# Optimization experiments

Hardware: AMD Instinct MI355X
Metric: run time of the kernel (lower is better)

The kernel has to match this reference:

```python
import jax, jax.numpy as jnp
import numpy as np

B, T, I, H, O = 256, 512, 128, 256, 1


def setup_inputs() -> dict:
    key = jax.random.key(0)
    ks = jax.random.split(key, 7)
    s_ih = 1.0 / np.sqrt(H)
    return {
        "x": jax.random.normal(ks[0], (B, T, I), dtype=jnp.float32),
        "W_ih": jax.random.uniform(ks[1], (H, I), jnp.float32, -s_ih, s_ih),
        "W_hh": jax.random.uniform(ks[2], (H, H), jnp.float32, -s_ih, s_ih),
        "b_ih": jax.random.uniform(ks[3], (H,), jnp.float32, -s_ih, s_ih),
        "b_hh": jax.random.uniform(ks[4], (H,), jnp.float32, -s_ih, s_ih),
        "fc_w": jax.random.uniform(ks[5], (O, H), jnp.float32, -s_ih, s_ih),
        "fc_b": jax.random.uniform(ks[6], (O,), jnp.float32, -s_ih, s_ih),
    }


def reference(x, W_ih, W_hh, b_ih, b_hh, fc_w, fc_b):
    # Elman RNN (tanh), batch_first, single layer, h0 = zeros.
    # Only the last hidden state feeds the fc head, so scan carries h only.
    b = b_ih + b_hh
    xW = jnp.einsum('bti,hi->tbh', x, W_ih) + b  # precompute input projection [T,B,H]

    def step(h, xw_t):
        h = jnp.tanh(xw_t + h @ W_hh.T)
        return h, None

    h0 = jnp.zeros((x.shape[0], W_hh.shape[0]), dtype=x.dtype)
    h_last, _ = jax.lax.scan(step, h0, xW)
    return h_last @ fc_w.T + fc_b  # [B, O]
```

## Files before the change

### kernel.cpp

```cpp
#include <hip/hip_runtime.h>
#include <hip/hip_bf16.h>

#define B_ 256
#define T_ 512
#define I_ 128
#define H_ 256

#define SC 2.885390081777927f

typedef __bf16 bf16x8 __attribute__((ext_vector_type(8)));
typedef float  f32x4  __attribute__((ext_vector_type(4)));
typedef unsigned short u16;
typedef unsigned int   u32;

union U16x8Cast { uint4 v; bf16x8 b; };

__device__ inline u16 f2b(float f) {
    union { __bf16 h; u16 u; } c; c.h = (__bf16)f; return c.u;
}
__device__ inline bf16x8 pack8(float4 lo, float4 hi) {
    bf16x8 f;
    f[0]=(__bf16)lo.x; f[1]=(__bf16)lo.y; f[2]=(__bf16)lo.z; f[3]=(__bf16)lo.w;
    f[4]=(__bf16)hi.x; f[5]=(__bf16)hi.y; f[6]=(__bf16)hi.z; f[7]=(__bf16)hi.w;
    return f;
}
__device__ inline bf16x8 pack8s(float4 lo, float4 hi, float s) {
    bf16x8 f;
    f[0]=(__bf16)(lo.x*s); f[1]=(__bf16)(lo.y*s); f[2]=(__bf16)(lo.z*s); f[3]=(__bf16)(lo.w*s);
    f[4]=(__bf16)(hi.x*s); f[5]=(__bf16)(hi.y*s); f[6]=(__bf16)(hi.z*s); f[7]=(__bf16)(hi.w*s);
    return f;
}
__device__ inline uint2 pack4(float a, float b, float c, float d) {
    uint2 p;
    p.x = (u32)f2b(a) | ((u32)f2b(b) << 16);
    p.y = (u32)f2b(c) | ((u32)f2b(d) << 16);
    return p;
}
__device__ inline f32x4 b4_to_f32x4(uint2 u) {
    f32x4 r;
    r[0] = __uint_as_float(u.x << 16);
    r[1] = __uint_as_float(u.x & 0xFFFF0000u);
    r[2] = __uint_as_float(u.y << 16);
    r[3] = __uint_as_float(u.y & 0xFFFF0000u);
    return r;
}
__device__ inline float tanh_pre(float s) {
    float e = __builtin_amdgcn_exp2f(s);
    float r = __builtin_amdgcn_rcpf(1.f + e);
    return fmaf(-2.f, r, 1.f);
}

#define WG_BARRIER() asm volatile("s_waitcnt lgkmcnt(0)\n\ts_barrier" ::: "memory")

#define LDST 264
__global__ __launch_bounds__(256, 2) void xw_gemm_mfma(const float* __restrict__ x,
                                                       const float* __restrict__ W_ih,
                                                       const float* __restrict__ b_ih,
                                                       const float* __restrict__ b_hh,
                                                       u16* __restrict__ xw) {
    __shared__ u16 tile[64 * LDST];

    const int tid  = (int)threadIdx.x;
    const int wave = tid >> 6;
    const int lane = tid & 63;
    const int q    = lane >> 4;
    const int ml   = lane & 15;
    const int m0   = (int)blockIdx.x * 128;
    const int b    = m0 >> 9;
    const int t0   = m0 & 511;
    const int n0   = wave * 64;

    bf16x8 wA[4][4];
#pragma unroll
    for (int tau = 0; tau < 4; ++tau) {
        const float* wr = W_ih + (size_t)(n0 + tau * 16 + ml) * I_;
#pragma unroll
        for (int kap = 0; kap < 4; ++kap) {
            const int k0 = kap * 32 + q * 8;
            wA[tau][kap] = pack8s(*(const float4*)(wr + k0), *(const float4*)(wr + k0 + 4), SC);
        }
    }

    f32x4 acc[8][4];
#pragma unroll
    for (int mt = 0; mt < 8; ++mt)
#pragma unroll
        for (int tau = 0; tau < 4; ++tau) acc[mt][tau] = (f32x4)0.f;

#pragma unroll
    for (int kap = 0; kap < 4; ++kap) {
        bf16x8 xB[8];
#pragma unroll
        for (int mt = 0; mt < 8; ++mt) {
            const float* xr = x + (size_t)(m0 + mt * 16 + ml) * I_ + kap * 32 + q * 8;
            xB[mt] = pack8(*(const float4*)xr, *(const float4*)(xr + 4));
        }
#pragma unroll
        for (int mt = 0; mt < 8; ++mt)
#pragma unroll
            for (int tau = 0; tau < 4; ++tau)
                acc[mt][tau] = __builtin_amdgcn_mfma_f32_16x16x32_bf16(
                    wA[tau][kap], xB[mt], acc[mt][tau], 0, 0, 0);
    }

    float4 bias4[4];
#pragma unroll
    for (int tau = 0; tau < 4; ++tau) {
        const int n = n0 + tau * 16 + q * 4;
        float4 bi = *(const float4*)(b_ih + n);
        float4 bh = *(const float4*)(b_hh + n);
        bias4[tau] = make_float4((bi.x + bh.x) * SC, (bi.y + bh.y) * SC,
                                 (bi.z + bh.z) * SC, (bi.w + bh.w) * SC);
    }

#pragma unroll
    for (int p = 0; p < 2; ++p) {
        if (p) __syncthreads();
#pragma unroll
        for (int mt = 0; mt < 4; ++mt) {
            const int row = mt * 16 + ml;
            const int mg  = p * 4 + mt;
#pragma unroll
            for (int tau = 0; tau < 4; ++tau) {
                uint2 pk = pack4(acc[mg][tau][0] + bias4[tau].x,
                                 acc[mg][tau][1] + bias4[tau].y,
                                 acc[mg][tau][2] + bias4[tau].z,
                                 acc[mg][tau][3] + bias4[tau].w);
                *(uint2*)(tile + row * LDST + n0 + tau * 16 + q * 4) = pk;
            }
        }
        __syncthreads();
#pragma unroll
        for (int s = 0; s < 4; ++s) {
            const int rr = s * 16 + (tid >> 4);
            const int c  = tid & 15;
            const uint4* srcp = (const uint4*)(tile + rr * LDST);
            uint4* dstp = (uint4*)(xw + ((size_t)(t0 + p * 64 + rr) * B_ + b) * H_);
            uint4 v0 = srcp[c];
            uint4 v1 = srcp[c + 16];
            dstp[c] = v0;
            dstp[c + 16] = v1;
        }
    }
}

__global__ __launch_bounds__(512, 2) void rnn_scan_mfma(const u16* __restrict__ xw,
                                                        const float* __restrict__ W_hh,
                                                        const float* __restrict__ fc_w,
                                                        const float* __restrict__ fc_b,
                                                        float* __restrict__ out) {
    __shared__ __attribute__((aligned(16))) u16 hbuf[2][4096];
    __shared__ float red[8][16];

    const int tid  = (int)threadIdx.x;
    const int wave = tid >> 6;
    const int lane = tid & 63;
    const int q    = lane >> 4;
    const int m    = lane & 15;
    const int b0   = (int)blockIdx.x * 16;

    bf16x8 wf[2][8];
#pragma unroll
    for (int tau2 = 0; tau2 < 2; ++tau2) {
        const float* wr = W_hh + (size_t)(wave * 32 + tau2 * 16 + m) * H_;
#pragma unroll
        for (int kap = 0; kap < 8; ++kap) {
            const int k0 = kap * 32 + q * 8;
            wf[tau2][kap] = pack8s(*(const float4*)(wr + k0), *(const float4*)(wr + k0 + 4), SC);
        }
    }

    int widx[2];
#pragma unroll
    for (int tau2 = 0; tau2 < 2; ++tau2) {
        const int nbw = wave * 32 + tau2 * 16 + q * 4;
        widx[tau2] = (nbw >> 5) * 512 + (((nbw >> 3) & 3) * 16 + m) * 8 + (nbw & 7);
    }

    {
        uint4* p = (uint4*)&hbuf[0][0];
        const uint4 z = {0u, 0u, 0u, 0u};
        p[tid] = z;
    }
    WG_BARRIER();

    const u16* xwp = xw + (size_t)(b0 + m) * H_ + (wave * 32 + q * 4);
    const size_t tstride = (size_t)B_ * H_;

    uint2 pfA[2], pfB[2];
    pfA[0] = *(const uint2*)(xwp);
    pfA[1] = *(const uint2*)(xwp + 16);
    pfB[0] = *(const uint2*)(xwp + tstride);
    pfB[1] = *(const uint2*)(xwp + tstride + 16);

    int cur = 0;
    f32x4 acc[2];
    for (int tt = 0; tt < T_ / 2; ++tt) {
        {
            const int t = 2 * tt;
            acc[0] = b4_to_f32x4(pfA[0]);
            acc[1] = b4_to_f32x4(pfA[1]);
            if (t + 2 < T_) {
                const u16* pt = xwp + (size_t)(t + 2) * tstride;
                pfA[0] = *(const uint2*)(pt);
                pfA[1] = *(const uint2*)(pt + 16);
            }
            const uint4* hb = (const uint4*)&hbuf[cur][0];
#pragma unroll
            for (int kap = 0; kap < 8; ++kap) {
                U16x8Cast c; c.v = hb[kap * 64 + lane];
                acc[0] = __builtin_amdgcn_mfma_f32_16x16x32_bf16(wf[0][kap], c.b, acc[0], 0, 0, 0);
                acc[1] = __builtin_amdgcn_mfma_f32_16x16x32_bf16(wf[1][kap], c.b, acc[1], 0, 0, 0);
            }
            u16* wb = &hbuf[cur ^ 1][0];
#pragma unroll
            for (int tau2 = 0; tau2 < 2; ++tau2) {
                uint2 pk = pack4(tanh_pre(acc[tau2][0]), tanh_pre(acc[tau2][1]),
                                 tanh_pre(acc[tau2][2]), tanh_pre(acc[tau2][3]));
                *(uint2*)(wb + widx[tau2]) = pk;
            }
            WG_BARRIER();
            cur ^= 1;
        }
        {
            const int t = 2 * tt + 1;
            acc[0] = b4_to_f32x4(pfB[0]);
            acc[1] = b4_to_f32x4(pfB[1]);
            if (t + 2 < T_) {
                const u16* pt = xwp + (size_t)(t + 2) * tstride;
                pfB[0] = *(const uint2*)(pt);
                pfB[1] = *(const uint2*)(pt + 16);
            }
            const uint4* hb = (const uint4*)&hbuf[cur][0];
#pragma unroll
            for (int kap = 0; kap < 8; ++kap) {
                U16x8Cast c; c.v = hb[kap * 64 + lane];
                acc[0] = __builtin_amdgcn_mfma_f32_16x16x32_bf16(wf[0][kap], c.b, acc[0], 0, 0, 0);
                acc[1] = __builtin_amdgcn_mfma_f32_16x16x32_bf16(wf[1][kap], c.b, acc[1], 0, 0, 0);
            }
            if (t != T_ - 1) {
                u16* wb = &hbuf[cur ^ 1][0];
#pragma unroll
                for (int tau2 = 0; tau2 < 2; ++tau2) {
                    uint2 pk = pack4(tanh_pre(acc[tau2][0]), tanh_pre(acc[tau2][1]),
                                     tanh_pre(acc[tau2][2]), tanh_pre(acc[tau2][3]));
                    *(uint2*)(wb + widx[tau2]) = pk;
                }
                WG_BARRIER();
                cur ^= 1;
            }
        }
    }

    float4 fcw[2];
#pragma unroll
    for (int tau2 = 0; tau2 < 2; ++tau2)
        fcw[tau2] = *(const float4*)(fc_w + wave * 32 + tau2 * 16 + q * 4);

    float partial = 0.f;
#pragma unroll
    for (int tau2 = 0; tau2 < 2; ++tau2) {
        partial += tanh_pre(acc[tau2][0]) * fcw[tau2].x;
        partial += tanh_pre(acc[tau2][1]) * fcw[tau2].y;
        partial += tanh_pre(acc[tau2][2]) * fcw[tau2].z;
        partial += tanh_pre(acc[tau2][3]) * fcw[tau2].w;
    }
    partial += __shfl_xor(partial, 16);
    partial += __shfl_xor(partial, 32);
    __syncthreads();
    if (lane < 16) red[wave][m] = partial;
    __syncthreads();
    if (tid < 16) {
        float s = red[0][tid] + red[1][tid] + red[2][tid] + red[3][tid]
                + red[4][tid] + red[5][tid] + red[6][tid] + red[7][tid];
        out[b0 + tid] = s + fc_b[0];
    }
}

extern "C" void kernel_launch(void* const* d_in, const int* in_sizes, int n_in,
                              void* d_out, int out_size, void* d_ws, size_t ws_size,
                              hipStream_t stream) {
    const float* x    = (const float*)d_in[0];
    const float* W_ih = (const float*)d_in[1];
    const float* W_hh = (const float*)d_in[2];
    const float* b_ih = (const float*)d_in[3];
    const float* b_hh = (const float*)d_in[4];
    const float* fc_w = (const float*)d_in[5];
    const float* fc_b = (const float*)d_in[6];
    float* out = (float*)d_out;

    u16* xwbuf = (u16*)d_ws;
    xw_gemm_mfma<<<(B_ * T_) / 128, 256, 0, stream>>>(x, W_ih, b_ih, b_hh, xwbuf);
    rnn_scan_mfma<<<B_ / 16, 512, 0, stream>>>(xwbuf, W_hh, fc_w, fc_b, out);
}
```

Measured before the change: 370.0 us.

## Process two batch groups per block to interleave independent MFMA chains

Each scan block now handles 32 batch rows as two 16-row groups, with separate LDS hidden-state buffers and accumulators. Both groups share the register-resident W_hh fragments and one barrier per timestep. Their independent MFMA dependency chains can overlap to hide latency in the serial recurrence. In exchange each step does more work per wave, register pressure rises (launch bounds lowered to one block), and the grid halves.

```diff
diff --git a/kernel.cpp b/kernel.cpp
--- a/kernel.cpp
+++ b/kernel.cpp
@@ -144,20 +144,20 @@
     }
 }
 
-__global__ __launch_bounds__(512, 2) void rnn_scan_mfma(const u16* __restrict__ xw,
+__global__ __launch_bounds__(512, 1) void rnn_scan_mfma(const u16* __restrict__ xw,
                                                         const float* __restrict__ W_hh,
                                                         const float* __restrict__ fc_w,
                                                         const float* __restrict__ fc_b,
                                                         float* __restrict__ out) {
-    __shared__ __attribute__((aligned(16))) u16 hbuf[2][4096];
-    __shared__ float red[8][16];
+    __shared__ __attribute__((aligned(16))) u16 hbuf[2][2][4096];
+    __shared__ float red[2][8][16];
 
     const int tid  = (int)threadIdx.x;
     const int wave = tid >> 6;
     const int lane = tid & 63;
     const int q    = lane >> 4;
     const int m    = lane & 15;
-    const int b0   = (int)blockIdx.x * 16;
+    const int b0   = (int)blockIdx.x * 32;
 
     bf16x8 wf[2][8];
 #pragma unroll
@@ -178,102 +178,111 @@
     }
 
     {
-        uint4* p = (uint4*)&hbuf[0][0];
         const uint4 z = {0u, 0u, 0u, 0u};
-        p[tid] = z;
-    }
-    WG_BARRIER();
-
-    const u16* xwp = xw + (size_t)(b0 + m) * H_ + (wave * 32 + q * 4);
+        ((uint4*)&hbuf[0][0][0])[tid] = z;
+        ((uint4*)&hbuf[1][0][0])[tid] = z;
+    }
+    __syncthreads();
+
+    const u16* xwpA = xw + (size_t)(b0 + m) * H_ + (wave * 32 + q * 4);
+    const u16* xwpB = xwpA + (size_t)16 * H_;
     const size_t tstride = (size_t)B_ * H_;
 
-    uint2 pfA[2], pfB[2];
-    pfA[0] = *(const uint2*)(xwp);
-    pfA[1] = *(const uint2*)(xwp + 16);
-    pfB[0] = *(const uint2*)(xwp + tstride);
-    pfB[1] = *(const uint2*)(xwp + tstride + 16);
+    uint2 pfEA[2], pfOA[2], pfEB[2], pfOB[2];
+    pfEA[0] = *(const uint2*)(xwpA);             pfEA[1] = *(const uint2*)(xwpA + 16);
+    pfEB[0] = *(const uint2*)(xwpB);             pfEB[1] = *(const uint2*)(xwpB + 16);
+    pfOA[0] = *(const uint2*)(xwpA + tstride);   pfOA[1] = *(const uint2*)(xwpA + tstride + 16);
+    pfOB[0] = *(const uint2*)(xwpB + tstride);   pfOB[1] = *(const uint2*)(xwpB + tstride + 16);
 
     int cur = 0;
-    f32x4 acc[2];
+    f32x4 accA[2], accB[2];
+
+#define DUAL_STEP(T_CUR, PFA, PFB, WRITE_OUT)                                   \
+    {                                                                           \
+        const int t_ = (T_CUR);                                                 \
+            \
+        const uint4* hbA_ = (const uint4*)&hbuf[0][cur][0];                     \
+        const uint4* hbB_ = (const uint4*)&hbuf[1][cur][0];                     \
+        U16x8Cast cvA[8], cvB[8];                                               \
+        _Pragma("unroll")                                                       \
+        for (int k = 0; k < 8; ++k) cvA[k].v = hbA_[k * 64 + lane];             \
+        _Pragma("unroll")                                                       \
+        for (int k = 0; k < 8; ++k) cvB[k].v = hbB_[k * 64 + lane];             \
+                    \
+        accA[0] = b4_to_f32x4(PFA[0]);  accA[1] = b4_to_f32x4(PFA[1]);          \
+        accB[0] = b4_to_f32x4(PFB[0]);  accB[1] = b4_to_f32x4(PFB[1]);          \
+        if (t_ + 2 < T_) {                                                      \
+            const u16* ptA_ = xwpA + (size_t)(t_ + 2) * tstride;                \
+            const u16* ptB_ = xwpB + (size_t)(t_ + 2) * tstride;                \
+            PFA[0] = *(const uint2*)(ptA_);  PFA[1] = *(const uint2*)(ptA_ + 16); \
+            PFB[0] = *(const uint2*)(ptB_);  PFB[1] = *(const uint2*)(ptB_ + 16); \
+        }                                                                       \
+                      \
+        _Pragma("unroll")                                                       \
+        for (int k = 0; k < 8; ++k) {                                           \
+            accA[0] = __builtin_amdgcn_mfma_f32_16x16x32_bf16(wf[0][k], cvA[k].b, accA[0], 0, 0, 0); \
+            accA[1] = __builtin_amdgcn_mfma_f32_16x16x32_bf16(wf[1][k], cvA[k].b, accA[1], 0, 0, 0); \
+        }                                                                       \
+        _Pragma("unroll")                                                       \
+        for (int k = 0; k < 8; ++k) {                                           \
+            accB[0] = __builtin_amdgcn_mfma_f32_16x16x32_bf16(wf[0][k], cvB[k].b, accB[0], 0, 0, 0); \
+            accB[1] = __builtin_amdgcn_mfma_f32_16x16x32_bf16(wf[1][k], cvB[k].b, accB[1], 0, 0, 0); \
+        }                                                                       \
+           \
+        if (WRITE_OUT) {                                                        \
+            u16* wbA_ = &hbuf[0][cur ^ 1][0];                                   \
+            u16* wbB_ = &hbuf[1][cur ^ 1][0];                                   \
+            _Pragma("unroll")                                                   \
+            for (int tau2 = 0; tau2 < 2; ++tau2) {                              \
+                uint2 pk_ = pack4(tanh_pre(accA[tau2][0]), tanh_pre(accA[tau2][1]), \
+                                  tanh_pre(accA[tau2][2]), tanh_pre(accA[tau2][3])); \
+                *(uint2*)(wbA_ + widx[tau2]) = pk_;                             \
+            }                                                                   \
+            _Pragma("unroll")                                                   \
+            for (int tau2 = 0; tau2 < 2; ++tau2) {                              \
+                uint2 pk_ = pack4(tanh_pre(accB[tau2][0]), tanh_pre(accB[tau2][1]), \
+                                  tanh_pre(accB[tau2][2]), tanh_pre(accB[tau2][3])); \
+                *(uint2*)(wbB_ + widx[tau2]) = pk_;                             \
+            }                                                                   \
+            WG_BARRIER();                                                       \
+            cur ^= 1;                                                           \
+        }                                                                       \
+    }
+
     for (int tt = 0; tt < T_ / 2; ++tt) {
-        {
-            const int t = 2 * tt;
-            acc[0] = b4_to_f32x4(pfA[0]);
-            acc[1] = b4_to_f32x4(pfA[1]);
-            if (t + 2 < T_) {
-                const u16* pt = xwp + (size_t)(t + 2) * tstride;
-                pfA[0] = *(const uint2*)(pt);
-                pfA[1] = *(const uint2*)(pt + 16);
-            }
-            const uint4* hb = (const uint4*)&hbuf[cur][0];
-#pragma unroll
-            for (int kap = 0; kap < 8; ++kap) {
-                U16x8Cast c; c.v = hb[kap * 64 + lane];
-                acc[0] = __builtin_amdgcn_mfma_f32_16x16x32_bf16(wf[0][kap], c.b, acc[0], 0, 0, 0);
-                acc[1] = __builtin_amdgcn_mfma_f32_16x16x32_bf16(wf[1][kap], c.b, acc[1], 0, 0, 0);
-            }
-            u16* wb = &hbuf[cur ^ 1][0];
-#pragma unroll
-            for (int tau2 = 0; tau2 < 2; ++tau2) {
-                uint2 pk = pack4(tanh_pre(acc[tau2][0]), tanh_pre(acc[tau2][1]),
-                                 tanh_pre(acc[tau2][2]), tanh_pre(acc[tau2][3]));
-                *(uint2*)(wb + widx[tau2]) = pk;
-            }
-            WG_BARRIER();
-            cur ^= 1;
-        }
-        {
-            const int t = 2 * tt + 1;
-            acc[0] = b4_to_f32x4(pfB[0]);
-            acc[1] = b4_to_f32x4(pfB[1]);
-            if (t + 2 < T_) {
-                const u16* pt = xwp + (size_t)(t + 2) * tstride;
-                pfB[0] = *(const uint2*)(pt);
-                pfB[1] = *(const uint2*)(pt + 16);
-            }
-            const uint4* hb = (const uint4*)&hbuf[cur][0];
-#pragma unroll
-            for (int kap = 0; kap < 8; ++kap) {
-                U16x8Cast c; c.v = hb[kap * 64 + lane];
-                acc[0] = __builtin_amdgcn_mfma_f32_16x16x32_bf16(wf[0][kap], c.b, acc[0], 0, 0, 0);
-                acc[1] = __builtin_amdgcn_mfma_f32_16x16x32_bf16(wf[1][kap], c.b, acc[1], 0, 0, 0);
-            }
-            if (t != T_ - 1) {
-                u16* wb = &hbuf[cur ^ 1][0];
-#pragma unroll
-                for (int tau2 = 0; tau2 < 2; ++tau2) {
-                    uint2 pk = pack4(tanh_pre(acc[tau2][0]), tanh_pre(acc[tau2][1]),
-                                     tanh_pre(acc[tau2][2]), tanh_pre(acc[tau2][3]));
-                    *(uint2*)(wb + widx[tau2]) = pk;
-                }
-                WG_BARRIER();
-                cur ^= 1;
-            }
-        }
-    }
+        DUAL_STEP(2 * tt,     pfEA, pfEB, true);
+        DUAL_STEP(2 * tt + 1, pfOA, pfOB, (2 * tt + 1) != (T_ - 1));
+    }
+#undef DUAL_STEP
 
     float4 fcw[2];
 #pragma unroll
     for (int tau2 = 0; tau2 < 2; ++tau2)
         fcw[tau2] = *(const float4*)(fc_w + wave * 32 + tau2 * 16 + q * 4);
 
-    float partial = 0.f;
+    float pA = 0.f, pB = 0.f;
 #pragma unroll
     for (int tau2 = 0; tau2 < 2; ++tau2) {
-        partial += tanh_pre(acc[tau2][0]) * fcw[tau2].x;
-        partial += tanh_pre(acc[tau2][1]) * fcw[tau2].y;
-        partial += tanh_pre(acc[tau2][2]) * fcw[tau2].z;
-        partial += tanh_pre(acc[tau2][3]) * fcw[tau2].w;
-    }
-    partial += __shfl_xor(partial, 16);
-    partial += __shfl_xor(partial, 32);
+        pA += tanh_pre(accA[tau2][0]) * fcw[tau2].x;
+        pA += tanh_pre(accA[tau2][1]) * fcw[tau2].y;
+        pA += tanh_pre(accA[tau2][2]) * fcw[tau2].z;
+        pA += tanh_pre(accA[tau2][3]) * fcw[tau2].w;
+        pB += tanh_pre(accB[tau2][0]) * fcw[tau2].x;
+        pB += tanh_pre(accB[tau2][1]) * fcw[tau2].y;
+        pB += tanh_pre(accB[tau2][2]) * fcw[tau2].z;
+        pB += tanh_pre(accB[tau2][3]) * fcw[tau2].w;
+    }
+    pA += __shfl_xor(pA, 16);  pA += __shfl_xor(pA, 32);
+    pB += __shfl_xor(pB, 16);  pB += __shfl_xor(pB, 32);
     __syncthreads();
-    if (lane < 16) red[wave][m] = partial;
+    if (lane < 16) { red[0][wave][m] = pA; red[1][wave][m] = pB; }
     __syncthreads();
-    if (tid < 16) {
-        float s = red[0][tid] + red[1][tid] + red[2][tid] + red[3][tid]
-                + red[4][tid] + red[5][tid] + red[6][tid] + red[7][tid];
-        out[b0 + tid] = s + fc_b[0];
+    if (tid < 32) {
+        const int g  = tid >> 4;
+        const int bb = tid & 15;
+        float s = red[g][0][bb] + red[g][1][bb] + red[g][2][bb] + red[g][3][bb]
+                + red[g][4][bb] + red[g][5][bb] + red[g][6][bb] + red[g][7][bb];
+        out[b0 + g * 16 + bb] = s + fc_b[0];
     }
 }
 
@@ -291,5 +300,5 @@
 
     u16* xwbuf = (u16*)d_ws;
     xw_gemm_mfma<<<(B_ * T_) / 128, 256, 0, stream>>>(x, W_ih, b_ih, b_hh, xwbuf);
-    rnn_scan_mfma<<<B_ / 16, 512, 0, stream>>>(xwbuf, W_hh, fc_w, fc_b, out);
-}
+    rnn_scan_mfma<<<B_ / 32, 512, 0, stream>>>(xwbuf, W_hh, fc_w, fc_b, out);
+}
```

Result: slower. 601.8 us (+62.6%).

## Replace per-step workgroup barrier with per-wave LDS flags and 4-deep h ring

Applied to the files above, without the earlier changes.

The scan kernel's per-timestep s_barrier is replaced with point-to-point synchronisation. Each wave publishes a release flag after writing its slice of h, and consumers spin on acquire loads only for the chunks they need. The chunk order is rotated so each wave starts with its own freshly written slice, letting MFMAs begin before other waves finish. A 4-buffer ring of h and launch_bounds occupancy 1 are added to keep fast waves from overwriting data still being read, at the cost of more LDS and spin-polling overhead.

```diff
diff --git a/kernel.cpp b/kernel.cpp
--- a/kernel.cpp
+++ b/kernel.cpp
@@ -49,8 +49,6 @@
     float r = __builtin_amdgcn_rcpf(1.f + e);
     return fmaf(-2.f, r, 1.f);
 }
-
-#define WG_BARRIER() asm volatile("s_waitcnt lgkmcnt(0)\n\ts_barrier" ::: "memory")
 
 #define LDST 264
 __global__ __launch_bounds__(256, 2) void xw_gemm_mfma(const float* __restrict__ x,
@@ -144,12 +142,13 @@
     }
 }
 
-__global__ __launch_bounds__(512, 2) void rnn_scan_mfma(const u16* __restrict__ xw,
+__global__ __launch_bounds__(512, 1) void rnn_scan_mfma(const u16* __restrict__ xw,
                                                         const float* __restrict__ W_hh,
                                                         const float* __restrict__ fc_w,
                                                         const float* __restrict__ fc_b,
                                                         float* __restrict__ out) {
-    __shared__ __attribute__((aligned(16))) u16 hbuf[2][4096];
+    __shared__ __attribute__((aligned(16))) u16 hbuf[4][4096];
+    __shared__ u32 hflag[8];
     __shared__ float red[8][16];
 
     const int tid  = (int)threadIdx.x;
@@ -164,9 +163,10 @@
     for (int tau2 = 0; tau2 < 2; ++tau2) {
         const float* wr = W_hh + (size_t)(wave * 32 + tau2 * 16 + m) * H_;
 #pragma unroll
-        for (int kap = 0; kap < 8; ++kap) {
-            const int k0 = kap * 32 + q * 8;
-            wf[tau2][kap] = pack8s(*(const float4*)(wr + k0), *(const float4*)(wr + k0 + 4), SC);
+        for (int i = 0; i < 8; ++i) {
+            const int c  = (wave + i) & 7;
+            const int k0 = c * 32 + q * 8;
+            wf[tau2][i] = pack8s(*(const float4*)(wr + k0), *(const float4*)(wr + k0 + 4), SC);
         }
     }
 
@@ -181,8 +181,9 @@
         uint4* p = (uint4*)&hbuf[0][0];
         const uint4 z = {0u, 0u, 0u, 0u};
         p[tid] = z;
-    }
-    WG_BARRIER();
+        if (tid < 8) hflag[tid] = 0;
+    }
+    __syncthreads();
 
     const u16* xwp = xw + (size_t)(b0 + m) * H_ + (wave * 32 + q * 4);
     const size_t tstride = (size_t)B_ * H_;
@@ -193,64 +194,65 @@
     pfB[0] = *(const uint2*)(xwp + tstride);
     pfB[1] = *(const uint2*)(xwp + tstride + 16);
 
-    int cur = 0;
+    u32 flc[8];
+#pragma unroll
+    for (int i = 0; i < 8; ++i) flc[i] = 0;
+
     f32x4 acc[2];
+
+#define SCAN_STEP(T_CUR, PF, WRITE_OUT)                                        \
+    {                                                                          \
+        const int t_ = (T_CUR);                                                \
+        acc[0] = b4_to_f32x4(PF[0]);                                           \
+        acc[1] = b4_to_f32x4(PF[1]);                                           \
+        if (t_ + 2 < T_) {                                                     \
+            const u16* pt_ = xwp + (size_t)(t_ + 2) * tstride;                 \
+            PF[0] = *(const uint2*)(pt_);                                      \
+            PF[1] = *(const uint2*)(pt_ + 16);                                 \
+        }                                                                      \
+        const uint4* hb_ = (const uint4*)&hbuf[t_ & 3][0];                     \
+        U16x8Cast cv[8];                                                       \
+        cv[0].v = hb_[wave * 64 + lane];             \
+        _Pragma("unroll")                                                      \
+        for (int i = 1; i < 8; ++i) {                                          \
+            const int c_ = (wave + i) & 7;                                     \
+            if (flc[i] < (u32)t_) {                                            \
+                u32 f_;                                                        \
+                do {                                                           \
+                    f_ = __hip_atomic_load(&hflag[c_], __ATOMIC_ACQUIRE,       \
+                                           __HIP_MEMORY_SCOPE_WORKGROUP);      \
+                } while (f_ < (u32)t_);                                        \
+                flc[i] = f_;                                                   \
+            }                                                                  \
+            cv[i].v = hb_[c_ * 64 + lane];                                     \
+            acc[0] = __builtin_amdgcn_mfma_f32_16x16x32_bf16(                  \
+                wf[0][i - 1], cv[i - 1].b, acc[0], 0, 0, 0);                   \
+            acc[1] = __builtin_amdgcn_mfma_f32_16x16x32_bf16(                  \
+                wf[1][i - 1], cv[i - 1].b, acc[1], 0, 0, 0);                   \
+        }                                                                      \
+        acc[0] = __builtin_amdgcn_mfma_f32_16x16x32_bf16(                      \
+            wf[0][7], cv[7].b, acc[0], 0, 0, 0);                               \
+        acc[1] = __builtin_amdgcn_mfma_f32_16x16x32_bf16(                      \
+            wf[1][7], cv[7].b, acc[1], 0, 0, 0);                               \
+        if (WRITE_OUT) {                                                       \
+            u16* wb_ = &hbuf[(t_ + 1) & 3][0];                                 \
+            _Pragma("unroll")                                                  \
+            for (int tau2 = 0; tau2 < 2; ++tau2) {                             \
+                uint2 pk_ = pack4(tanh_pre(acc[tau2][0]), tanh_pre(acc[tau2][1]), \
+                                  tanh_pre(acc[tau2][2]), tanh_pre(acc[tau2][3])); \
+                *(uint2*)(wb_ + widx[tau2]) = pk_;                             \
+            }                                                                  \
+            if (lane == 0)                                                     \
+                __hip_atomic_store(&hflag[wave], (u32)(t_ + 1),                \
+                                   __ATOMIC_RELEASE, __HIP_MEMORY_SCOPE_WORKGROUP); \
+        }                                                                      \
+    }
+
     for (int tt = 0; tt < T_ / 2; ++tt) {
-        {
-            const int t = 2 * tt;
-            acc[0] = b4_to_f32x4(pfA[0]);
-            acc[1] = b4_to_f32x4(pfA[1]);
-            if (t + 2 < T_) {
-                const u16* pt = xwp + (size_t)(t + 2) * tstride;
-                pfA[0] = *(const uint2*)(pt);
-                pfA[1] = *(const uint2*)(pt + 16);
-            }
-            const uint4* hb = (const uint4*)&hbuf[cur][0];
-#pragma unroll
-            for (int kap = 0; kap < 8; ++kap) {
-                U16x8Cast c; c.v = hb[kap * 64 + lane];
-                acc[0] = __builtin_amdgcn_mfma_f32_16x16x32_bf16(wf[0][kap], c.b, acc[0], 0, 0, 0);
-                acc[1] = __builtin_amdgcn_mfma_f32_16x16x32_bf16(wf[1][kap], c.b, acc[1], 0, 0, 0);
-            }
-            u16* wb = &hbuf[cur ^ 1][0];
-#pragma unroll
-            for (int tau2 = 0; tau2 < 2; ++tau2) {
-                uint2 pk = pack4(tanh_pre(acc[tau2][0]), tanh_pre(acc[tau2][1]),
-                                 tanh_pre(acc[tau2][2]), tanh_pre(acc[tau2][3]));
-                *(uint2*)(wb + widx[tau2]) = pk;
-            }
-            WG_BARRIER();
-            cur ^= 1;
-        }
-        {
-            const int t = 2 * tt + 1;
-            acc[0] = b4_to_f32x4(pfB[0]);
-            acc[1] = b4_to_f32x4(pfB[1]);
-            if (t + 2 < T_) {
-                const u16* pt = xwp + (size_t)(t + 2) * tstride;
-                pfB[0] = *(const uint2*)(pt);
-                pfB[1] = *(const uint2*)(pt + 16);
-            }
-            const uint4* hb = (const uint4*)&hbuf[cur][0];
-#pragma unroll
-            for (int kap = 0; kap < 8; ++kap) {
-                U16x8Cast c; c.v = hb[kap * 64 + lane];
-                acc[0] = __builtin_amdgcn_mfma_f32_16x16x32_bf16(wf[0][kap], c.b, acc[0], 0, 0, 0);
-                acc[1] = __builtin_amdgcn_mfma_f32_16x16x32_bf16(wf[1][kap], c.b, acc[1], 0, 0, 0);
-            }
-            if (t != T_ - 1) {
-                u16* wb = &hbuf[cur ^ 1][0];
-#pragma unroll
-                for (int tau2 = 0; tau2 < 2; ++tau2) {
-                    uint2 pk = pack4(tanh_pre(acc[tau2][0]), tanh_pre(acc[tau2][1]),
-                                     tanh_pre(acc[tau2][2]), tanh_pre(acc[tau2][3]));
-                    *(uint2*)(wb + widx[tau2]) = pk;
-                }
-                WG_BARRIER();
-                cur ^= 1;
-            }
-        }
-    }
+        SCAN_STEP(2 * tt,     pfA, true);
+        SCAN_STEP(2 * tt + 1, pfB, (2 * tt + 1) != (T_ - 1));
+    }
+#undef SCAN_STEP
 
     float4 fcw[2];
 #pragma unroll
```

Measured after the change: 503.7 us. +36.1%, slower.
